# Kernel tuning notes

Measured on AMD Instinct MI355X. Metric: run time of the kernel, lower is better.

The kernel has to match this reference:

```python
import math
import jax
import jax.numpy as jnp
import numpy as np

# --- static problem constants (match init_kwargs / input_specs) ---
B = 8            # number of point clouds
N = 4096         # points per cloud
RATIO = 0.25     # fps ratio -> m1 = ceil(RATIO*N) samples per cloud
K = 16           # kNN neighbors
OVERLAP = 0.2    # overlap_ratio


def setup_inputs() -> dict:
    key = jax.random.key(0)
    pos = jax.random.normal(key, (B * N, 3), dtype=jnp.float32)
    batch = jnp.repeat(jnp.arange(B, dtype=jnp.int32), N)  # sorted cloud ids, equal-sized clouds
    return {"pos": pos, "batch": batch}


def _fps_single(p, m):
    """Farthest point sampling on one cloud p:[N,3], returns m local indices (int32).
    Deterministic start at index 0; each step picks argmax of running min-distance."""
    n = p.shape[0]

    def step(carry, _):
        mind, last = carry
        d = jnp.sum((p - p[last]) ** 2, axis=-1)      # [N] sq-dist to last pick
        mind = jnp.minimum(mind, d)
        nxt = jnp.argmax(mind).astype(jnp.int32)
        return (mind, nxt), nxt

    init = (jnp.full((n,), jnp.inf, dtype=p.dtype), jnp.int32(0))
    _, picks = jax.lax.scan(step, init, None, length=m - 1)
    return jnp.concatenate([jnp.zeros((1,), jnp.int32), picks])


def _forward(pos, batch):
    pos_b = pos.reshape(B, N, 3)                       # equal-sized clouds
    m1 = math.ceil(RATIO * N)                          # base samples per cloud
    m2 = math.ceil(OVERLAP * N)                        # extra-fps samples per cloud
    offs = (jnp.arange(B, dtype=jnp.int32) * N)[:, None]

    base_idx = (jax.vmap(lambda p: _fps_single(p, m1))(pos_b) + offs).reshape(-1)   # [B*m1]
    extra_idx = (jax.vmap(lambda p: _fps_single(p, m2))(pos_b) + offs).reshape(-1)  # [B*m2]

    overlap_size = int(B * m1 * OVERLAP)
    combined_idx = jnp.concatenate([base_idx, extra_idx[:overlap_size]])            # [M]

    # batched kNN: each query searches only within its own cloud
    qb = combined_idx // N                             # query cloud id == batch[combined_idx]
    qpos = pos[combined_idx]                           # [M,3]
    d = jnp.sum((qpos[:, None, :] - pos_b[qb]) ** 2, axis=-1)  # [M,N] sq-dists within cloud
    _, nn_local = jax.lax.top_k(-d, K)                 # [M,K] nearest local indices
    col = (qb[:, None] * N + nn_local.astype(jnp.int32)).reshape(-1)  # global source indices
    row = jnp.repeat(jnp.arange(combined_idx.shape[0], dtype=jnp.int32), K)
    return combined_idx, row, col


def reference(pos, batch):
    return _forward(pos, batch)
```

## Files before the change

### kernel.cpp

```cpp
#include <hip/hip_runtime.h>
#include <math.h>

#define NPTS   4096
#define NB     8
#define M1     1024
#define M2     820
#define NEXTRA 1638
#define MQ     9830
#define KK     16

typedef unsigned int u32;
typedef unsigned long long u64;
typedef float f32x2 __attribute__((ext_vector_type(2)));

#define DPP_MAX(CTRL) do {                                                         \
    u32 olo_ = (u32)__builtin_amdgcn_update_dpp((int)klo_, (int)klo_, CTRL, 0xF, 0xF, false); \
    u32 ohi_ = (u32)__builtin_amdgcn_update_dpp((int)khi_, (int)khi_, CTRL, 0xF, 0xF, false); \
    u64 ok_ = ((u64)ohi_ << 32) | olo_;                                            \
    u64 ck_ = ((u64)khi_ << 32) | klo_;                                            \
    if (ok_ > ck_) { klo_ = olo_; khi_ = ohi_; }                                   \
} while (0)

#define DPP_MIN(CTRL) do {                                                         \
    u32 olo_ = (u32)__builtin_amdgcn_update_dpp((int)klo_, (int)klo_, CTRL, 0xF, 0xF, false); \
    u32 ohi_ = (u32)__builtin_amdgcn_update_dpp((int)khi_, (int)khi_, CTRL, 0xF, 0xF, false); \
    u64 ok_ = ((u64)ohi_ << 32) | olo_;                                            \
    u64 ck_ = ((u64)khi_ << 32) | klo_;                                            \
    if (ok_ < ck_) { klo_ = olo_; khi_ = ohi_; }                                   \
} while (0)

__global__ __launch_bounds__(256) void fps_kernel(const float* __restrict__ pos,
                                                  int* __restrict__ picks) {
#pragma clang fp contract(off)
    __shared__ float sx[NPTS], sy[NPTS], sz[NPTS];
    __shared__ u32 slo[2][4], shi[2][4];
    const int b = blockIdx.x;
    const int t = threadIdx.x;
    const float* cp = pos + (size_t)b * NPTS * 3;
    for (int i = t; i < NPTS * 3; i += 256) {
        float v = cp[i];
        int p = i / 3, c = i - p * 3;
        if (c == 0) sx[p] = v;
        else if (c == 1) sy[p] = v;
        else sz[p] = v;
    }
    __syncthreads();

    f32x2 X[8], Y[8], Z[8], MD[8];
    u32 klo[16];
#pragma unroll
    for (int r = 0; r < 8; ++r) {
        int p0 = (2 * r) * 256 + t, p1 = p0 + 256;
        X[r] = f32x2{sx[p0], sx[p1]};
        Y[r] = f32x2{sy[p0], sy[p1]};
        Z[r] = f32x2{sz[p0], sz[p1]};
        MD[r] = f32x2{__builtin_inff(), __builtin_inff()};
    }
#pragma unroll
    for (int j = 0; j < 16; ++j) klo[j] = ~(u32)(j * 256 + t);

    if (t == 0) picks[b * M1] = 0;
    float xl = sx[0], yl = sy[0], zl = sz[0];
    const int wave = t >> 6;

    for (int s = 1; s < M1; ++s) {
        const int par = s & 1;
        const f32x2 xl2 = f32x2{xl, xl};
        const f32x2 yl2 = f32x2{yl, yl};
        const f32x2 zl2 = f32x2{zl, zl};
        u64 kk[16];
#pragma unroll
        for (int r = 0; r < 8; ++r) {
            f32x2 dx = X[r] - xl2;
            f32x2 dy = Y[r] - yl2;
            f32x2 dz = Z[r] - zl2;
            f32x2 d = (dx * dx + dy * dy) + dz * dz;
            f32x2 m = __builtin_elementwise_min(MD[r], d);
            MD[r] = m;
            kk[2 * r]     = ((u64)__float_as_uint(m[0]) << 32) | klo[2 * r];
            kk[2 * r + 1] = ((u64)__float_as_uint(m[1]) << 32) | klo[2 * r + 1];
        }
#pragma unroll
        for (int st = 8; st >= 1; st >>= 1) {
#pragma unroll
            for (int i = 0; i < 16; ++i) {
                if (i < st) { if (kk[i + st] > kk[i]) kk[i] = kk[i + st]; }
            }
        }
        u32 klo_ = (u32)kk[0], khi_ = (u32)(kk[0] >> 32);
        DPP_MAX(0x121); DPP_MAX(0x122); DPP_MAX(0x124); DPP_MAX(0x128);
        DPP_MAX(0x142); DPP_MAX(0x143);
        u32 wlo = (u32)__builtin_amdgcn_readlane((int)klo_, 63);
        u32 whi = (u32)__builtin_amdgcn_readlane((int)khi_, 63);
        if ((t & 63) == 0) { slo[par][wave] = wlo; shi[par][wave] = whi; }
        __syncthreads();
        u64 bk = ((u64)shi[par][0] << 32) | slo[par][0];
#pragma unroll
        for (int wv = 1; wv < 4; ++wv) {
            u64 ok = ((u64)shi[par][wv] << 32) | slo[par][wv];
            if (ok > bk) bk = ok;
        }
        const int best = (int)(~(u32)bk);
        xl = sx[best]; yl = sy[best]; zl = sz[best];
        if (t == 0) picks[b * M1 + s] = best;
    }
}

__global__ __launch_bounds__(256) void build_kernel(const int* __restrict__ picks,
                                                    int* __restrict__ out) {
    int i = blockIdx.x * 256 + threadIdx.x;
    if (i < MQ) {
        int v;
        if (i < NB * M1) {
            int b = i >> 10;
            v = b * NPTS + picks[i];
        } else {
            int e = i - NB * M1;
            int b = e / M2;
            int j = e - b * M2;
            v = b * NPTS + picks[b * M1 + j];
        }
        out[i] = v;
    }
    if (i < MQ * KK) {
        out[MQ + i] = i >> 4;
    }
}

__global__ __launch_bounds__(256) void knn_kernel(const float* __restrict__ pos,
                                                  int* __restrict__ out) {
#pragma clang fp contract(off)
    const int q = blockIdx.x * 4 + (threadIdx.x >> 6);
    const int l = threadIdx.x & 63;
    if (q >= MQ) return;
    const int cidx = out[q];
    const int qb = cidx >> 12;
    const float qx = pos[(size_t)cidx * 3 + 0];
    const float qy = pos[(size_t)cidx * 3 + 1];
    const float qz = pos[(size_t)cidx * 3 + 2];
    const float* cp = pos + (size_t)qb * NPTS * 3;
    float D[64];
    float lv = __builtin_inff(); int li = 0;
#pragma unroll
    for (int j = 0; j < 64; ++j) {
        int p = j * 64 + l;
        float dx = cp[p * 3 + 0] - qx;
        float dy = cp[p * 3 + 1] - qy;
        float dz = cp[p * 3 + 2] - qz;
        float d = dx * dx + dy * dy + dz * dz;
        D[j] = d;
        if (d < lv) { lv = d; li = p; }
    }
    unsigned long long mask = 0;
    int* colout = out + MQ + MQ * KK + q * KK;
    for (int r = 0; r < KK; ++r) {
        u32 klo_ = (u32)li, khi_ = __float_as_uint(lv);
        DPP_MIN(0x121); DPP_MIN(0x122); DPP_MIN(0x124); DPP_MIN(0x128);
        DPP_MIN(0x142); DPP_MIN(0x143);
        u32 bi = (u32)__builtin_amdgcn_readlane((int)klo_, 63);
        if (l == 0) colout[r] = qb * NPTS + (int)bi;
        if ((bi & 63) == (u32)l) mask |= 1ull << (bi >> 6);
        lv = __builtin_inff(); li = 0;
#pragma unroll
        for (int j = 0; j < 64; ++j) {
            bool act = ((mask >> j) & 1ull) == 0ull;
            float d = D[j];
            if (act && d < lv) { lv = d; li = j * 64 + l; }
        }
    }
}

extern "C" void kernel_launch(void* const* d_in, const int* in_sizes, int n_in,
                              void* d_out, int out_size, void* d_ws, size_t ws_size,
                              hipStream_t stream) {
    const float* pos = (const float*)d_in[0];
    int* picks = (int*)d_ws;
    int* out = (int*)d_out;
    fps_kernel<<<NB, 256, 0, stream>>>(pos, picks);
    build_kernel<<<(MQ * KK + 255) / 256, 256, 0, stream>>>(picks, out);
    knn_kernel<<<(MQ + 3) / 4, 256, 0, stream>>>(pos, out);
}
```

Baseline: 785.7 us.

## Restructure FPS step reduction: float-keyed tree, per-wave winner coords, lighter barrier

The per-thread argmax now runs over 32-bit floats with small slot indices instead of 64-bit packed keys. The lane that owns each wave's winner writes that point's coordinates to shared memory, so the dependent LDS gather of the chosen point after the barrier goes away. The barrier becomes an inline s_waitcnt+s_barrier, and picks are buffered in LDS and written to global memory once at the end. This shortens the serial critical path of each of the 1023 dependent steps. It adds a register switch and risks tie-breaking differences if equal distances are ordered differently in the per-thread reduction.

```diff
diff --git a/kernel.cpp b/kernel.cpp
--- a/kernel.cpp
+++ b/kernel.cpp
@@ -1,5 +1,4 @@
 #include <hip/hip_runtime.h>
-#include <math.h>
 
 #define NPTS   4096
 #define NB     8
@@ -33,7 +32,9 @@
                                                   int* __restrict__ picks) {
 #pragma clang fp contract(off)
     __shared__ float sx[NPTS], sy[NPTS], sz[NPTS];
-    __shared__ u32 slo[2][4], shi[2][4];
+    __shared__ int sp[M1];
+    __shared__ u64 skey[2][4];
+    __shared__ float sxw[2][4], syw[2][4], szw[2][4];
     const int b = blockIdx.x;
     const int t = threadIdx.x;
     const float* cp = pos + (size_t)b * NPTS * 3;
@@ -44,10 +45,10 @@
         else if (c == 1) sy[p] = v;
         else sz[p] = v;
     }
+    if (t == 0) sp[0] = 0;
     __syncthreads();
 
     f32x2 X[8], Y[8], Z[8], MD[8];
-    u32 klo[16];
 #pragma unroll
     for (int r = 0; r < 8; ++r) {
         int p0 = (2 * r) * 256 + t, p1 = p0 + 256;
@@ -56,10 +57,6 @@
         Z[r] = f32x2{sz[p0], sz[p1]};
         MD[r] = f32x2{__builtin_inff(), __builtin_inff()};
     }
-#pragma unroll
-    for (int j = 0; j < 16; ++j) klo[j] = ~(u32)(j * 256 + t);
-
-    if (t == 0) picks[b * M1] = 0;
     float xl = sx[0], yl = sy[0], zl = sz[0];
     const int wave = t >> 6;
 
@@ -68,7 +65,8 @@
         const f32x2 xl2 = f32x2{xl, xl};
         const f32x2 yl2 = f32x2{yl, yl};
         const f32x2 zl2 = f32x2{zl, zl};
-        u64 kk[16];
+        float mv[16];
+        int mj[16];
 #pragma unroll
         for (int r = 0; r < 8; ++r) {
             f32x2 dx = X[r] - xl2;
@@ -77,33 +75,55 @@
             f32x2 d = (dx * dx + dy * dy) + dz * dz;
             f32x2 m = __builtin_elementwise_min(MD[r], d);
             MD[r] = m;
-            kk[2 * r]     = ((u64)__float_as_uint(m[0]) << 32) | klo[2 * r];
-            kk[2 * r + 1] = ((u64)__float_as_uint(m[1]) << 32) | klo[2 * r + 1];
+            mv[2 * r] = m[0];     mj[2 * r] = 2 * r;
+            mv[2 * r + 1] = m[1]; mj[2 * r + 1] = 2 * r + 1;
         }
 #pragma unroll
         for (int st = 8; st >= 1; st >>= 1) {
 #pragma unroll
             for (int i = 0; i < 16; ++i) {
-                if (i < st) { if (kk[i + st] > kk[i]) kk[i] = kk[i + st]; }
+                if (i < st) {
+                    if (mv[i + st] > mv[i]) { mv[i] = mv[i + st]; mj[i] = mj[i + st]; }
+                }
             }
         }
-        u32 klo_ = (u32)kk[0], khi_ = (u32)(kk[0] >> 32);
+        u32 klo_ = ~(u32)((mj[0] << 8) + t);
+        u32 khi_ = __float_as_uint(mv[0]);
         DPP_MAX(0x121); DPP_MAX(0x122); DPP_MAX(0x124); DPP_MAX(0x128);
         DPP_MAX(0x142); DPP_MAX(0x143);
-        u32 wlo = (u32)__builtin_amdgcn_readlane((int)klo_, 63);
-        u32 whi = (u32)__builtin_amdgcn_readlane((int)khi_, 63);
-        if ((t & 63) == 0) { slo[par][wave] = wlo; shi[par][wave] = whi; }
-        __syncthreads();
-        u64 bk = ((u64)shi[par][0] << 32) | slo[par][0];
-#pragma unroll
-        for (int wv = 1; wv < 4; ++wv) {
-            u64 ok = ((u64)shi[par][wv] << 32) | slo[par][wv];
-            if (ok > bk) bk = ok;
-        }
-        const int best = (int)(~(u32)bk);
-        xl = sx[best]; yl = sy[best]; zl = sz[best];
-        if (t == 0) picks[b * M1 + s] = best;
-    }
+        if ((t & 63) == 63) skey[par][wave] = ((u64)khi_ << 32) | klo_;
+        const int idx = (int)~(u32)__builtin_amdgcn_readlane((int)klo_, 63);
+        const int j = idx >> 8;
+        f32x2 xp, yp, zp;
+        switch (j >> 1) {
+            case 0: xp = X[0]; yp = Y[0]; zp = Z[0]; break;
+            case 1: xp = X[1]; yp = Y[1]; zp = Z[1]; break;
+            case 2: xp = X[2]; yp = Y[2]; zp = Z[2]; break;
+            case 3: xp = X[3]; yp = Y[3]; zp = Z[3]; break;
+            case 4: xp = X[4]; yp = Y[4]; zp = Z[4]; break;
+            case 5: xp = X[5]; yp = Y[5]; zp = Z[5]; break;
+            case 6: xp = X[6]; yp = Y[6]; zp = Z[6]; break;
+            default: xp = X[7]; yp = Y[7]; zp = Z[7]; break;
+        }
+        const int h = j & 1;
+        if ((idx & 255) == t) {
+            sxw[par][wave] = h ? xp[1] : xp[0];
+            syw[par][wave] = h ? yp[1] : yp[0];
+            szw[par][wave] = h ? zp[1] : zp[0];
+        }
+        asm volatile("s_waitcnt lgkmcnt(0)\n\ts_barrier" ::: "memory");
+        u64 k0 = skey[par][0], k1 = skey[par][1], k2 = skey[par][2], k3 = skey[par][3];
+        float x0 = sxw[par][0], x1 = sxw[par][1], x2 = sxw[par][2], x3 = sxw[par][3];
+        float y0 = syw[par][0], y1 = syw[par][1], y2 = syw[par][2], y3 = syw[par][3];
+        float z0 = szw[par][0], z1 = szw[par][1], z2 = szw[par][2], z3 = szw[par][3];
+        u64 bk = k0; xl = x0; yl = y0; zl = z0;
+        if (k1 > bk) { bk = k1; xl = x1; yl = y1; zl = z1; }
+        if (k2 > bk) { bk = k2; xl = x2; yl = y2; zl = z2; }
+        if (k3 > bk) { bk = k3; xl = x3; yl = y3; zl = z3; }
+        if (t == 0) sp[s] = (int)~(u32)bk;
+    }
+    __syncthreads();
+    for (int i = t; i < M1; i += 256) picks[b * M1 + i] = sp[i];
 }
 
 __global__ __launch_bounds__(256) void build_kernel(const int* __restrict__ picks,
```

Measured after the change: 1.020 ms. +29.8%, slower.

## Shorten FPS serial step: 32-bit local argmax, broadcast winner coords via LDS

Applied to the files above, without the earlier changes.

Each thread now reduces its 16 candidates with 32-bit float compares and a slot index instead of 64-bit packed keys. The wave-winning lane writes its key and coordinates to LDS, with non-winners writing to private scratch so no branch is needed. After the barrier, every thread reads the new point's coordinates directly, which removes the dependent sx/sy/sz lookup after the cross-wave reduction. Picks are buffered in shared memory and written to global once at the end. Tie-breaking changes: within a thread the lower index wins ties, which matches the original inverted-index ordering.

```diff
diff --git a/kernel.cpp b/kernel.cpp
--- a/kernel.cpp
+++ b/kernel.cpp
@@ -1,5 +1,4 @@
 #include <hip/hip_runtime.h>
-#include <math.h>
 
 #define NPTS   4096
 #define NB     8
@@ -33,7 +32,8 @@
                                                   int* __restrict__ picks) {
 #pragma clang fp contract(off)
     __shared__ float sx[NPTS], sy[NPTS], sz[NPTS];
-    __shared__ u32 slo[2][4], shi[2][4];
+    __shared__ int sp[M1];
+    __shared__ float sbuf[64 + 256 * 8];
     const int b = blockIdx.x;
     const int t = threadIdx.x;
     const float* cp = pos + (size_t)b * NPTS * 3;
@@ -44,10 +44,10 @@
         else if (c == 1) sy[p] = v;
         else sz[p] = v;
     }
+    if (t == 0) sp[0] = 0;
     __syncthreads();
 
     f32x2 X[8], Y[8], Z[8], MD[8];
-    u32 klo[16];
 #pragma unroll
     for (int r = 0; r < 8; ++r) {
         int p0 = (2 * r) * 256 + t, p1 = p0 + 256;
@@ -56,19 +56,17 @@
         Z[r] = f32x2{sz[p0], sz[p1]};
         MD[r] = f32x2{__builtin_inff(), __builtin_inff()};
     }
-#pragma unroll
-    for (int j = 0; j < 16; ++j) klo[j] = ~(u32)(j * 256 + t);
-
-    if (t == 0) picks[b * M1] = 0;
     float xl = sx[0], yl = sy[0], zl = sz[0];
     const int wave = t >> 6;
+    const int scrOff = 64 + t * 8;
 
     for (int s = 1; s < M1; ++s) {
         const int par = s & 1;
         const f32x2 xl2 = f32x2{xl, xl};
         const f32x2 yl2 = f32x2{yl, yl};
         const f32x2 zl2 = f32x2{zl, zl};
-        u64 kk[16];
+        float wv[8];
+        int ws[8];
 #pragma unroll
         for (int r = 0; r < 8; ++r) {
             f32x2 dx = X[r] - xl2;
@@ -77,33 +75,53 @@
             f32x2 d = (dx * dx + dy * dy) + dz * dz;
             f32x2 m = __builtin_elementwise_min(MD[r], d);
             MD[r] = m;
-            kk[2 * r]     = ((u64)__float_as_uint(m[0]) << 32) | klo[2 * r];
-            kk[2 * r + 1] = ((u64)__float_as_uint(m[1]) << 32) | klo[2 * r + 1];
-        }
-#pragma unroll
-        for (int st = 8; st >= 1; st >>= 1) {
-#pragma unroll
-            for (int i = 0; i < 16; ++i) {
-                if (i < st) { if (kk[i + st] > kk[i]) kk[i] = kk[i + st]; }
+            bool c = m[1] > m[0];
+            wv[r] = c ? m[1] : m[0];
+            ws[r] = c ? 2 * r + 1 : 2 * r;
+        }
+#pragma unroll
+        for (int st = 4; st >= 1; st >>= 1) {
+#pragma unroll
+            for (int i = 0; i < 8; ++i) {
+                if (i < st) {
+                    if (wv[i + st] > wv[i]) { wv[i] = wv[i + st]; ws[i] = ws[i + st]; }
+                }
             }
         }
-        u32 klo_ = (u32)kk[0], khi_ = (u32)(kk[0] >> 32);
+        const int ci = (ws[0] << 8) + t;
+        const float cx = sx[ci], cy = sy[ci], cz = sz[ci];
+        u32 klo_ = ~(u32)ci;
+        u32 khi_ = __float_as_uint(wv[0]);
+        const u32 mylo = klo_, myhi = khi_;
         DPP_MAX(0x121); DPP_MAX(0x122); DPP_MAX(0x124); DPP_MAX(0x128);
         DPP_MAX(0x142); DPP_MAX(0x143);
-        u32 wlo = (u32)__builtin_amdgcn_readlane((int)klo_, 63);
-        u32 whi = (u32)__builtin_amdgcn_readlane((int)khi_, 63);
-        if ((t & 63) == 0) { slo[par][wave] = wlo; shi[par][wave] = whi; }
+        const u32 swlo = (u32)__builtin_amdgcn_readlane((int)klo_, 63);
+        const int off = (mylo == swlo) ? ((par * 4 + wave) * 8) : scrOff;
+        float4 pay;
+        pay.x = __uint_as_float(mylo); pay.y = __uint_as_float(myhi);
+        pay.z = cx; pay.w = cy;
+        *(float4*)&sbuf[off] = pay;
+        sbuf[off + 4] = cz;
         __syncthreads();
-        u64 bk = ((u64)shi[par][0] << 32) | slo[par][0];
-#pragma unroll
-        for (int wv = 1; wv < 4; ++wv) {
-            u64 ok = ((u64)shi[par][wv] << 32) | slo[par][wv];
-            if (ok > bk) bk = ok;
-        }
-        const int best = (int)(~(u32)bk);
-        xl = sx[best]; yl = sy[best]; zl = sz[best];
-        if (t == 0) picks[b * M1 + s] = best;
-    }
+        const int sb = par * 32;
+        const float4 a0 = *(const float4*)&sbuf[sb + 0];  const float z0 = sbuf[sb + 4];
+        const float4 a1 = *(const float4*)&sbuf[sb + 8];  const float z1 = sbuf[sb + 12];
+        const float4 a2 = *(const float4*)&sbuf[sb + 16]; const float z2 = sbuf[sb + 20];
+        const float4 a3 = *(const float4*)&sbuf[sb + 24]; const float z3 = sbuf[sb + 28];
+        u64 k0 = ((u64)__float_as_uint(a0.y) << 32) | __float_as_uint(a0.x);
+        u64 k1 = ((u64)__float_as_uint(a1.y) << 32) | __float_as_uint(a1.x);
+        u64 k2 = ((u64)__float_as_uint(a2.y) << 32) | __float_as_uint(a2.x);
+        u64 k3 = ((u64)__float_as_uint(a3.y) << 32) | __float_as_uint(a3.x);
+        u64 ka = k0; float xa = a0.z, ya = a0.w, za = z0;
+        if (k1 > ka) { ka = k1; xa = a1.z; ya = a1.w; za = z1; }
+        u64 kb = k2; float xb = a2.z, yb = a2.w, zb = z2;
+        if (k3 > kb) { kb = k3; xb = a3.z; yb = a3.w; zb = z3; }
+        if (kb > ka) { ka = kb; xa = xb; ya = yb; za = zb; }
+        xl = xa; yl = ya; zl = za;
+        if (t == 0) sp[s] = (int)~(u32)ka;
+    }
+    __syncthreads();
+    for (int i = t; i < M1; i += 256) picks[b * M1 + i] = sp[i];
 }
 
 __global__ __launch_bounds__(256) void build_kernel(const int* __restrict__ picks,
```

New measurement: 798.6 us. No clear change (+1.6%).

## Replace FPS block barrier with flag-tagged LDS slots and lighter argmax

Applied to the files above, without the earlier changes.

Inside each FPS step, the per-thread argmax now runs on floats with small register indices instead of 64-bit packed keys. The winning lane of each wave publishes its candidate's coordinates and key into LDS slots tagged with the step number. All threads spin on these volatile slots instead of calling __syncthreads, so the block barrier and the dependent coordinate lookup are removed from the critical serial loop. The cost is spin-polling LDS traffic, and correctness now depends on the tags being seen in order, with a step-tagged parity double buffer guarding reuse.

```diff
diff --git a/kernel.cpp b/kernel.cpp
--- a/kernel.cpp
+++ b/kernel.cpp
@@ -1,11 +1,9 @@
 #include <hip/hip_runtime.h>
-#include <math.h>
 
 #define NPTS   4096
 #define NB     8
 #define M1     1024
 #define M2     820
-#define NEXTRA 1638
 #define MQ     9830
 #define KK     16
 
@@ -33,7 +31,7 @@
                                                   int* __restrict__ picks) {
 #pragma clang fp contract(off)
     __shared__ float sx[NPTS], sy[NPTS], sz[NPTS];
-    __shared__ u32 slo[2][4], shi[2][4];
+    __shared__ __align__(16) u32 slots[2][4][8];
     const int b = blockIdx.x;
     const int t = threadIdx.x;
     const float* cp = pos + (size_t)b * NPTS * 3;
@@ -44,10 +42,11 @@
         else if (c == 1) sy[p] = v;
         else sz[p] = v;
     }
+    if (t < 64) ((u32*)slots)[t] = 0xFFFFFFFFu;
+    if (t == 0) picks[b * M1] = 0;
     __syncthreads();
 
     f32x2 X[8], Y[8], Z[8], MD[8];
-    u32 klo[16];
 #pragma unroll
     for (int r = 0; r < 8; ++r) {
         int p0 = (2 * r) * 256 + t, p1 = p0 + 256;
@@ -56,10 +55,6 @@
         Z[r] = f32x2{sz[p0], sz[p1]};
         MD[r] = f32x2{__builtin_inff(), __builtin_inff()};
     }
-#pragma unroll
-    for (int j = 0; j < 16; ++j) klo[j] = ~(u32)(j * 256 + t);
-
-    if (t == 0) picks[b * M1] = 0;
     float xl = sx[0], yl = sy[0], zl = sz[0];
     const int wave = t >> 6;
 
@@ -68,7 +63,8 @@
         const f32x2 xl2 = f32x2{xl, xl};
         const f32x2 yl2 = f32x2{yl, yl};
         const f32x2 zl2 = f32x2{zl, zl};
-        u64 kk[16];
+        float mv[8];
+        int mi[8];
 #pragma unroll
         for (int r = 0; r < 8; ++r) {
             f32x2 dx = X[r] - xl2;
@@ -77,32 +73,65 @@
             f32x2 d = (dx * dx + dy * dy) + dz * dz;
             f32x2 m = __builtin_elementwise_min(MD[r], d);
             MD[r] = m;
-            kk[2 * r]     = ((u64)__float_as_uint(m[0]) << 32) | klo[2 * r];
-            kk[2 * r + 1] = ((u64)__float_as_uint(m[1]) << 32) | klo[2 * r + 1];
-        }
-#pragma unroll
-        for (int st = 8; st >= 1; st >>= 1) {
-#pragma unroll
-            for (int i = 0; i < 16; ++i) {
-                if (i < st) { if (kk[i + st] > kk[i]) kk[i] = kk[i + st]; }
+            bool c = m[1] > m[0];
+            mv[r] = c ? m[1] : m[0];
+            mi[r] = c ? 2 * r + 1 : 2 * r;
+        }
+#pragma unroll
+        for (int st = 4; st >= 1; st >>= 1) {
+#pragma unroll
+            for (int i = 0; i < 8; ++i) {
+                if (i < st) {
+                    if (mv[i + st] > mv[i]) { mv[i] = mv[i + st]; mi[i] = mi[i + st]; }
+                }
             }
         }
-        u32 klo_ = (u32)kk[0], khi_ = (u32)(kk[0] >> 32);
+        const int ci = (mi[0] << 8) + t;
+        float cx = sx[ci], cy = sy[ci], cz = sz[ci];
+        __builtin_amdgcn_sched_barrier(0);
+        u32 klo_ = (((u32)(4095 - ci)) << 12) | (u32)s;
+        u32 khi_ = __float_as_uint(mv[0]);
+        const u32 mylo = klo_;
         DPP_MAX(0x121); DPP_MAX(0x122); DPP_MAX(0x124); DPP_MAX(0x128);
         DPP_MAX(0x142); DPP_MAX(0x143);
-        u32 wlo = (u32)__builtin_amdgcn_readlane((int)klo_, 63);
-        u32 whi = (u32)__builtin_amdgcn_readlane((int)khi_, 63);
-        if ((t & 63) == 0) { slo[par][wave] = wlo; shi[par][wave] = whi; }
-        __syncthreads();
-        u64 bk = ((u64)shi[par][0] << 32) | slo[par][0];
-#pragma unroll
-        for (int wv = 1; wv < 4; ++wv) {
-            u64 ok = ((u64)shi[par][wv] << 32) | slo[par][wv];
-            if (ok > bk) bk = ok;
-        }
-        const int best = (int)(~(u32)bk);
-        xl = sx[best]; yl = sy[best]; zl = sz[best];
-        if (t == 0) picks[b * M1 + s] = best;
+        const u32 wlo = (u32)__builtin_amdgcn_readlane((int)klo_, 63);
+        if (mylo == wlo) {
+            volatile u64* sl = (volatile u64*)&slots[par][wave][0];
+            const u64 st64 = (u64)(u32)s << 32;
+            sl[0] = st64 | __float_as_uint(cx);
+            sl[1] = st64 | __float_as_uint(cy);
+            sl[2] = st64 | __float_as_uint(cz);
+            sl[3] = ((u64)khi_ << 32) | mylo;
+        }
+        u64 xw0, yw0, zw0, kw0, xw1, yw1, zw1, kw1;
+        u64 xw2, yw2, zw2, kw2, xw3, yw3, zw3, kw3;
+        for (;;) {
+            volatile u64* s0 = (volatile u64*)&slots[par][0][0];
+            volatile u64* s1 = (volatile u64*)&slots[par][1][0];
+            volatile u64* s2 = (volatile u64*)&slots[par][2][0];
+            volatile u64* s3 = (volatile u64*)&slots[par][3][0];
+            xw0 = s0[0]; yw0 = s0[1]; zw0 = s0[2]; kw0 = s0[3];
+            xw1 = s1[0]; yw1 = s1[1]; zw1 = s1[2]; kw1 = s1[3];
+            xw2 = s2[0]; yw2 = s2[1]; zw2 = s2[2]; kw2 = s2[3];
+            xw3 = s3[0]; yw3 = s3[1]; zw3 = s3[2]; kw3 = s3[3];
+            const u32 us = (u32)s;
+            bool ok = ((u32)(xw0 >> 32) == us) & ((u32)(yw0 >> 32) == us) &
+                      ((u32)(zw0 >> 32) == us) & (((u32)kw0 & 0xFFFu) == us) &
+                      ((u32)(xw1 >> 32) == us) & ((u32)(yw1 >> 32) == us) &
+                      ((u32)(zw1 >> 32) == us) & (((u32)kw1 & 0xFFFu) == us) &
+                      ((u32)(xw2 >> 32) == us) & ((u32)(yw2 >> 32) == us) &
+                      ((u32)(zw2 >> 32) == us) & (((u32)kw2 & 0xFFFu) == us) &
+                      ((u32)(xw3 >> 32) == us) & ((u32)(yw3 >> 32) == us) &
+                      ((u32)(zw3 >> 32) == us) & (((u32)kw3 & 0xFFFu) == us);
+            if (ok) break;
+        }
+        u64 ka = kw0; u32 xa = (u32)xw0, ya = (u32)yw0, za = (u32)zw0;
+        if (kw1 > ka) { ka = kw1; xa = (u32)xw1; ya = (u32)yw1; za = (u32)zw1; }
+        u64 kb = kw2; u32 xb = (u32)xw2, yb = (u32)yw2, zb = (u32)zw2;
+        if (kw3 > kb) { kb = kw3; xb = (u32)xw3; yb = (u32)yw3; zb = (u32)zw3; }
+        if (kb > ka) { ka = kb; xa = xb; ya = yb; za = zb; }
+        xl = __uint_as_float(xa); yl = __uint_as_float(ya); zl = __uint_as_float(za);
+        if (t == 0) picks[b * M1 + s] = 4095 - (int)(((u32)ka) >> 12);
     }
 }
 
```

After: 1.475 ms. +87.7%, slower.
